# Kernel optimization log

Measured on AMD Instinct MI355X. Metric: run time of the kernel, lower is better.

The kernel has to match this reference:

```python
import jax, jax.numpy as jnp
import numpy as np

N_NODES = 100000


def gcn_conv(x, src, dst, dinv, W, b):
    # PyG GCNConv: h = D^-1/2 (A+I) D^-1/2 (x W) + b
    h = x @ W                                   # [N, out]
    norm = dinv[src] * dinv[dst]                # [E'] edge weights
    msg = norm[:, None] * h[src]                # gather + scale
    agg = jax.ops.segment_sum(msg, dst, num_segments=x.shape[0])
    return agg + b


def setup_inputs() -> dict:
    key = jax.random.key(0)
    ks = jax.random.split(key, 8)
    x = jax.random.normal(ks[0], (N_NODES, 64), dtype=jnp.float32)
    edge_index = jax.random.randint(ks[1], (2, 1600000), 0, N_NODES, dtype=jnp.int32)
    s = 0.1
    return {
        "x": x,
        "edge_index": edge_index,
        "W1": jax.random.normal(ks[2], (64, 64), dtype=jnp.float32) * s,
        "b1": jnp.zeros((64,), dtype=jnp.float32),
        "W2": jax.random.normal(ks[3], (64, 32), dtype=jnp.float32) * s,
        "b2": jnp.zeros((32,), dtype=jnp.float32),
        "W3": jax.random.normal(ks[4], (32, 2), dtype=jnp.float32) * s,
        "b3": jnp.zeros((2,), dtype=jnp.float32),
    }


def reference(x, edge_index, W1, b1, W2, b2, W3, b3):
    n = x.shape[0]
    loop = jnp.arange(n, dtype=edge_index.dtype)
    src = jnp.concatenate([edge_index[0], loop])  # add self-loops
    dst = jnp.concatenate([edge_index[1], loop])
    deg = jax.ops.segment_sum(jnp.ones_like(dst, dtype=x.dtype), dst, num_segments=n)
    dinv = jnp.where(deg > 0, jax.lax.rsqrt(jnp.maximum(deg, 1.0)), 0.0)
    h = jax.nn.relu(gcn_conv(x, src, dst, dinv, W1, b1))
    h = jax.nn.relu(gcn_conv(h, src, dst, dinv, W2, b2))
    return gcn_conv(h, src, dst, dinv, W3, b3)
```

## Files before the change

### kernel.cpp

```cpp
#include <hip/hip_runtime.h>
#include <hip/hip_fp16.h>

#define N_NODES 100000
#define N_EDGES 1600000
#define BSHIFT 9
#define NBUCK ((N_NODES + 511) / 512)
#define BCAP 12288

__global__ void bucket1_kernel(const int* __restrict__ src, const int* __restrict__ dst,
                               int* __restrict__ gbcount, int* __restrict__ bbuf, int E) {
    __shared__ int hcnt[NBUCK];
    __shared__ int hbase[NBUCK];
    int t = threadIdx.x;
    for (int i = t; i < NBUCK; i += 256) hcnt[i] = 0;
    __syncthreads();
    int e0 = blockIdx.x * 2048 + t;
    int ss[8], dd[8];
#pragma unroll
    for (int u = 0; u < 8; u++) {
        int e = e0 + u * 256;
        if (e < E) {
            ss[u] = src[e];
            dd[u] = dst[e];
            atomicAdd(&hcnt[dd[u] >> BSHIFT], 1);
        } else {
            dd[u] = -1;
        }
    }
    __syncthreads();
    for (int i = t; i < NBUCK; i += 256) {
        int c = hcnt[i];
        hbase[i] = c ? atomicAdd(&gbcount[i], c) : 0;
        hcnt[i] = 0;
    }
    __syncthreads();
#pragma unroll
    for (int u = 0; u < 8; u++) {
        if (dd[u] >= 0) {
            int bk = dd[u] >> BSHIFT;
            int r = atomicAdd(&hcnt[bk], 1);
            bbuf[(size_t)bk * BCAP + hbase[bk] + r] = ss[u] | ((dd[u] & 511) << 17);
        }
    }
}

__global__ void scan196_kernel(const int* __restrict__ gbcount, int* __restrict__ gbase,
                               int* __restrict__ rowptrN, int E) {
    __shared__ int s[256];
    int t = threadIdx.x;
    int v = (t < NBUCK) ? gbcount[t] : 0;
    s[t] = v;
    __syncthreads();
    for (int off = 1; off < 256; off <<= 1) {
        int u = (t >= off) ? s[t - off] : 0;
        __syncthreads();
        s[t] += u;
        __syncthreads();
    }
    if (t < NBUCK) gbase[t] = s[t] - v;
    if (t == 0) *rowptrN = E;
}

__global__ __launch_bounds__(512)
void bucket2_kernel(const int* __restrict__ bbuf, const int* __restrict__ gbcount,
                    const int* __restrict__ gbase, int* __restrict__ rowptr,
                    float* __restrict__ dinv, int* __restrict__ eidx, int N) {
    int b = blockIdx.x;
    int base_node = b << BSHIFT;
    int nn = min(512, N - base_node);
    int t = threadIdx.x;
    __shared__ int s[512];
    __shared__ int cur[512];
    s[t] = 0;
    __syncthreads();
    int sz = gbcount[b];
    const int* eb = bbuf + (size_t)b * BCAP;
    for (int j = t; j < sz; j += 512) atomicAdd(&s[((unsigned)eb[j]) >> 17], 1);
    __syncthreads();
    int myc = s[t];
    if (t < nn) dinv[base_node + t] = rsqrtf((float)myc + 1.0f);
    __syncthreads();
    for (int off = 1; off < 512; off <<= 1) {
        int u = (t >= off) ? s[t - off] : 0;
        __syncthreads();
        s[t] += u;
        __syncthreads();
    }
    int rp = gbase[b] + s[t] - myc;
    if (t < nn) rowptr[base_node + t] = rp;
    cur[t] = rp;
    __syncthreads();
    for (int j = t; j < sz; j += 512) {
        int e = eb[j];
        int pos = atomicAdd(&cur[((unsigned)e) >> 17], 1);
        eidx[pos] = e & 0x1FFFF;
    }
}

__global__ void sortrow_wave(const int* __restrict__ rowptr, int* __restrict__ eidx, int n) {
    int g = (blockIdx.x * blockDim.x + threadIdx.x) >> 6;
    int lane = threadIdx.x & 63;
    if (g >= n) return;
    int start = rowptr[g];
    int end = rowptr[g + 1];
    int len = end - start;
    if (len <= 1) return;

    if (len <= 64) {
        int v = (lane < len) ? eidx[start + lane] : 0x7fffffff;
#pragma unroll
        for (int k = 2; k <= 64; k <<= 1) {
#pragma unroll
            for (int j = k >> 1; j > 0; j >>= 1) {
                int partner = __shfl_xor(v, j, 64);
                bool up = ((lane & k) == 0);
                bool keepMin = (((lane & j) == 0) == up);
                int mn = min(v, partner), mx = max(v, partner);
                v = keepMin ? mn : mx;
            }
        }
        if (lane < len) eidx[start + lane] = v;
    } else if (lane == 0) {
        for (int i = start + 1; i < end; i++) {
            int key = eidx[i];
            int j = i - 1;
            while (j >= start && eidx[j] > key) { eidx[j + 1] = eidx[j]; j--; }
            eidx[j + 1] = key;
        }
    }
}

template <int FIN, int FOUT>
__global__ __launch_bounds__(256, 2)
void gemm_tiled(const float* __restrict__ in, const float* __restrict__ W,
                const float* __restrict__ dinv, __half* __restrict__ out, int n) {
    constexpr int CG = FOUT / 4;
    constexpr int RG = 256 / CG;
    constexpr int TR = RG * 4;
    constexpr int LDA = FIN + 4;
    __shared__ float sIn[TR * LDA];
    __shared__ float sW[FIN * FOUT];

    for (int i = threadIdx.x; i < FIN * FOUT / 4; i += 256)
        ((float4*)sW)[i] = ((const float4*)W)[i];

    int r0 = blockIdx.x * TR;
    for (int i = threadIdx.x; i < TR * FIN / 4; i += 256) {
        int rr = i / (FIN / 4);
        int cc = i % (FIN / 4);
        int gr = r0 + rr;
        float4 v = (gr < n) ? ((const float4*)in)[(size_t)gr * (FIN / 4) + cc]
                            : make_float4(0.f, 0.f, 0.f, 0.f);
        *(float4*)&sIn[rr * LDA + cc * 4] = v;
    }
    __syncthreads();

    int tc = threadIdx.x % CG;
    int tr = threadIdx.x / CG;
    int rbase = tr * 4, cbase = tc * 4;
    float acc[4][4] = {};

#pragma unroll 2
    for (int k = 0; k < FIN; k += 4) {
        float4 a[4], b[4];
#pragma unroll
        for (int i = 0; i < 4; i++) a[i] = *(float4*)&sIn[(rbase + i) * LDA + k];
#pragma unroll
        for (int kk = 0; kk < 4; kk++) b[kk] = *(float4*)&sW[(k + kk) * FOUT + cbase];
#pragma unroll
        for (int i = 0; i < 4; i++) {
            acc[i][0] += a[i].x * b[0].x + a[i].y * b[1].x + a[i].z * b[2].x + a[i].w * b[3].x;
            acc[i][1] += a[i].x * b[0].y + a[i].y * b[1].y + a[i].z * b[2].y + a[i].w * b[3].y;
            acc[i][2] += a[i].x * b[0].z + a[i].y * b[1].z + a[i].z * b[2].z + a[i].w * b[3].z;
            acc[i][3] += a[i].x * b[0].w + a[i].y * b[1].w + a[i].z * b[2].w + a[i].w * b[3].w;
        }
    }

#pragma unroll
    for (int i = 0; i < 4; i++) {
        int gr = r0 + rbase + i;
        if (gr < n) {
            float dv = dinv[gr];
            union { __half h[4]; uint2 u; } pk;
            pk.h[0] = __float2half_rn(dv * acc[i][0]);
            pk.h[1] = __float2half_rn(dv * acc[i][1]);
            pk.h[2] = __float2half_rn(dv * acc[i][2]);
            pk.h[3] = __float2half_rn(dv * acc[i][3]);
            *(uint2*)&out[(size_t)gr * FOUT + cbase] = pk.u;
        }
    }
}

__global__ __launch_bounds__(256, 4)
void agg_gemm64_kernel(const int* __restrict__ eidx, const int* __restrict__ rowptr,
                       const float* __restrict__ dinv, const __half* __restrict__ h,
                       const float* __restrict__ bias, const float* __restrict__ W,
                       __half* __restrict__ out, int n) {
    constexpr int FIN = 64, FOUT = 32;
    constexpr int L = 16;
    constexpr int PH = FIN / L;
    constexpr int NODES = 256 / L;
    constexpr int SVS = FIN + 1;
    using vh = _Float16 __attribute__((ext_vector_type(PH)));
    __shared__ float sW[FIN * FOUT];
    __shared__ float sv[NODES * SVS];

    for (int i = threadIdx.x; i < FIN * FOUT / 4; i += 256)
        ((float4*)sW)[i] = ((const float4*)W)[i];

    int g = (blockIdx.x * blockDim.x + threadIdx.x) / L;
    int lane = threadIdx.x % L;
    int slot = threadIdx.x / L;
    float di = 0.f;

    if (g < n) {
        int j = rowptr[g];
        int end = rowptr[g + 1];
        di = dinv[g];
        const __half* hb = h + lane * PH;

        float acc0[PH], acc1[PH];
#pragma unroll
        for (int q = 0; q < PH; q++) { acc0[q] = 0.f; acc1[q] = 0.f; }

        for (; j + 16 <= end; j += 16) {
            int s0 = eidx[j];
            int s1 = eidx[j + 1];
            int s2 = eidx[j + 2];
            int s3 = eidx[j + 3];
            int s4 = eidx[j + 4];
            int s5 = eidx[j + 5];
            int s6 = eidx[j + 6];
            int s7 = eidx[j + 7];
            vh v0 = *(const vh*)(hb + (size_t)s0 * FIN);
            vh v1 = *(const vh*)(hb + (size_t)s1 * FIN);
            vh v2 = *(const vh*)(hb + (size_t)s2 * FIN);
            vh v3 = *(const vh*)(hb + (size_t)s3 * FIN);
            vh v4 = *(const vh*)(hb + (size_t)s4 * FIN);
            vh v5 = *(const vh*)(hb + (size_t)s5 * FIN);
            vh v6 = *(const vh*)(hb + (size_t)s6 * FIN);
            vh v7 = *(const vh*)(hb + (size_t)s7 * FIN);
            int s8  = eidx[j + 8];
            int s9  = eidx[j + 9];
            int s10 = eidx[j + 10];
            int s11 = eidx[j + 11];
            int s12 = eidx[j + 12];
            int s13 = eidx[j + 13];
            int s14 = eidx[j + 14];
            int s15 = eidx[j + 15];
            vh v8  = *(const vh*)(hb + (size_t)s8  * FIN);
            vh v9  = *(const vh*)(hb + (size_t)s9  * FIN);
            vh v10 = *(const vh*)(hb + (size_t)s10 * FIN);
            vh v11 = *(const vh*)(hb + (size_t)s11 * FIN);
            vh v12 = *(const vh*)(hb + (size_t)s12 * FIN);
            vh v13 = *(const vh*)(hb + (size_t)s13 * FIN);
            vh v14 = *(const vh*)(hb + (size_t)s14 * FIN);
            vh v15 = *(const vh*)(hb + (size_t)s15 * FIN);
#pragma unroll
            for (int q = 0; q < PH; q++) {
                acc0[q] += (float)v0[q] + (float)v2[q];
                acc1[q] += (float)v1[q] + (float)v3[q];
                acc0[q] += (float)v4[q] + (float)v6[q];
                acc1[q] += (float)v5[q] + (float)v7[q];
            }
#pragma unroll
            for (int q = 0; q < PH; q++) {
                acc0[q] += (float)v8[q]  + (float)v10[q];
                acc1[q] += (float)v9[q]  + (float)v11[q];
                acc0[q] += (float)v12[q] + (float)v14[q];
                acc1[q] += (float)v13[q] + (float)v15[q];
            }
        }
        for (; j + 8 <= end; j += 8) {
            int s0 = eidx[j];
            int s1 = eidx[j + 1];
            int s2 = eidx[j + 2];
            int s3 = eidx[j + 3];
            int s4 = eidx[j + 4];
            int s5 = eidx[j + 5];
            int s6 = eidx[j + 6];
            int s7 = eidx[j + 7];
            vh v0 = *(const vh*)(hb + (size_t)s0 * FIN);
            vh v1 = *(const vh*)(hb + (size_t)s1 * FIN);
            vh v2 = *(const vh*)(hb + (size_t)s2 * FIN);
            vh v3 = *(const vh*)(hb + (size_t)s3 * FIN);
            vh v4 = *(const vh*)(hb + (size_t)s4 * FIN);
            vh v5 = *(const vh*)(hb + (size_t)s5 * FIN);
            vh v6 = *(const vh*)(hb + (size_t)s6 * FIN);
            vh v7 = *(const vh*)(hb + (size_t)s7 * FIN);
#pragma unroll
            for (int q = 0; q < PH; q++) {
                acc0[q] += (float)v0[q] + (float)v2[q];
                acc1[q] += (float)v1[q] + (float)v3[q];
                acc0[q] += (float)v4[q] + (float)v6[q];
                acc1[q] += (float)v5[q] + (float)v7[q];
            }
        }
        for (; j + 2 <= end; j += 2) {
            int s0 = eidx[j];
            int s1 = eidx[j + 1];
            vh v0 = *(const vh*)(hb + (size_t)s0 * FIN);
            vh v1 = *(const vh*)(hb + (size_t)s1 * FIN);
#pragma unroll
            for (int q = 0; q < PH; q++) { acc0[q] += (float)v0[q]; acc1[q] += (float)v1[q]; }
        }
        if (j < end) {
            vh v = *(const vh*)(hb + (size_t)eidx[j] * FIN);
#pragma unroll
            for (int q = 0; q < PH; q++) acc0[q] += (float)v[q];
        }

        vh sf = *(const vh*)(hb + (size_t)g * FIN);
        float* svn = &sv[slot * SVS + lane * PH];
#pragma unroll
        for (int q = 0; q < PH; q++) {
            float v = di * ((acc0[q] + acc1[q]) + (float)sf[q]) + bias[lane * PH + q];
            svn[q] = fmaxf(v, 0.f);
        }
    }
    __syncthreads();

    if (g < n) {
        const float* vn = &sv[slot * SVS];
        constexpr int PC = FOUT / L;
        float o0 = 0.f, o1 = 0.f;
        for (int k = 0; k < FIN; k++) {
            float vk = vn[k];
            float2 w = *(const float2*)&sW[k * FOUT + lane * PC];
            o0 += vk * w.x;
            o1 += vk * w.y;
        }
        union { __half h2[2]; unsigned u; } pk;
        pk.h2[0] = __float2half_rn(di * o0);
        pk.h2[1] = __float2half_rn(di * o1);
        *(unsigned*)&out[(size_t)g * FOUT + lane * PC] = pk.u;
    }
}

template <int FIN, int FOUT, bool OUT_HALF>
__global__ __launch_bounds__(256, 4)
void agg_gemm_kernel(const int* __restrict__ eidx, const int* __restrict__ rowptr,
                     const float* __restrict__ dinv, const __half* __restrict__ h,
                     const float* __restrict__ bias, const float* __restrict__ W,
                     void* __restrict__ outv, int n) {
    constexpr int L = 8;
    constexpr int PH = FIN / L;
    constexpr int NODES = 256 / L;
    constexpr int SVS = FIN + 1;
    using vh = _Float16 __attribute__((ext_vector_type(PH)));
    __shared__ float sW[FIN * FOUT];
    __shared__ float sv[NODES * SVS];

    for (int i = threadIdx.x; i < FIN * FOUT / 4; i += 256)
        ((float4*)sW)[i] = ((const float4*)W)[i];

    int g = (blockIdx.x * blockDim.x + threadIdx.x) / L;
    int lane = threadIdx.x % L;
    int slot = threadIdx.x / L;
    float di = 0.f;

    if (g < n) {
        int j = rowptr[g];
        int end = rowptr[g + 1];
        di = dinv[g];
        const __half* hb = h + lane * PH;

        float acc0[PH], acc1[PH];
#pragma unroll
        for (int q = 0; q < PH; q++) { acc0[q] = 0.f; acc1[q] = 0.f; }

        for (; j + 8 <= end; j += 8) {
            int s0 = eidx[j];
            int s1 = eidx[j + 1];
            int s2 = eidx[j + 2];
            int s3 = eidx[j + 3];
            int s4 = eidx[j + 4];
            int s5 = eidx[j + 5];
            int s6 = eidx[j + 6];
            int s7 = eidx[j + 7];
            vh v0 = *(const vh*)(hb + (size_t)s0 * FIN);
            vh v1 = *(const vh*)(hb + (size_t)s1 * FIN);
            vh v2 = *(const vh*)(hb + (size_t)s2 * FIN);
            vh v3 = *(const vh*)(hb + (size_t)s3 * FIN);
            vh v4 = *(const vh*)(hb + (size_t)s4 * FIN);
            vh v5 = *(const vh*)(hb + (size_t)s5 * FIN);
            vh v6 = *(const vh*)(hb + (size_t)s6 * FIN);
            vh v7 = *(const vh*)(hb + (size_t)s7 * FIN);
#pragma unroll
            for (int q = 0; q < PH; q++) {
                acc0[q] += (float)v0[q] + (float)v2[q];
                acc1[q] += (float)v1[q] + (float)v3[q];
                acc0[q] += (float)v4[q] + (float)v6[q];
                acc1[q] += (float)v5[q] + (float)v7[q];
            }
        }
        for (; j + 2 <= end; j += 2) {
            int s0 = eidx[j];
            int s1 = eidx[j + 1];
            vh v0 = *(const vh*)(hb + (size_t)s0 * FIN);
            vh v1 = *(const vh*)(hb + (size_t)s1 * FIN);
#pragma unroll
            for (int q = 0; q < PH; q++) { acc0[q] += (float)v0[q]; acc1[q] += (float)v1[q]; }
        }
        if (j < end) {
            vh v = *(const vh*)(hb + (size_t)eidx[j] * FIN);
#pragma unroll
            for (int q = 0; q < PH; q++) acc0[q] += (float)v[q];
        }

        vh sf = *(const vh*)(hb + (size_t)g * FIN);
        float* svn = &sv[slot * SVS + lane * PH];
#pragma unroll
        for (int q = 0; q < PH; q++) {
            float v = di * ((acc0[q] + acc1[q]) + (float)sf[q]) + bias[lane * PH + q];
            svn[q] = fmaxf(v, 0.f);
        }
    }
    __syncthreads();

    if (g < n) {
        const float* vn = &sv[slot * SVS];
        if constexpr (OUT_HALF) {
            constexpr int PC = FOUT / L;
            float o[PC] = {};
            for (int k = 0; k < FIN; k++) {
                float vk = vn[k];
                float4 w = *(const float4*)&sW[k * FOUT + lane * PC];
                o[0] += vk * w.x; o[1] += vk * w.y; o[2] += vk * w.z; o[3] += vk * w.w;
            }
            union { __half h[4]; uint2 u; } pk;
#pragma unroll
            for (int q = 0; q < PC; q++) pk.h[q] = __float2half_rn(di * o[q]);
            *(uint2*)((__half*)outv + (size_t)g * FOUT + lane * PC) = pk.u;
        } else {
            if (lane < FOUT) {
                float o = 0.f;
                for (int k = 0; k < FIN; k++) o += vn[k] * sW[k * FOUT + lane];
                ((float*)outv)[(size_t)g * FOUT + lane] = di * o;
            }
        }
    }
}

__global__ void agg2_kernel(const int* __restrict__ eidx, const int* __restrict__ rowptr,
                            const float* __restrict__ dinv, const float* __restrict__ h,
                            const float* __restrict__ b, float* __restrict__ out, int n) {
    int g = blockIdx.x * blockDim.x + threadIdx.x;
    if (g >= n) return;
    const float2* h2 = (const float2*)h;
    int j = rowptr[g];
    int end = rowptr[g + 1];
    float di = dinv[g];
    float2 hs = h2[g];

    float2 a0 = {0.f, 0.f}, a1 = {0.f, 0.f}, a2 = {0.f, 0.f}, a3 = {0.f, 0.f};
    float2 a4 = {0.f, 0.f}, a5 = {0.f, 0.f}, a6 = {0.f, 0.f}, a7 = {0.f, 0.f};
    for (; j + 8 <= end; j += 8) {
        int s0 = eidx[j];
        int s1 = eidx[j + 1];
        int s2 = eidx[j + 2];
        int s3 = eidx[j + 3];
        int s4 = eidx[j + 4];
        int s5 = eidx[j + 5];
        int s6 = eidx[j + 6];
        int s7 = eidx[j + 7];
        float2 v0 = h2[s0]; float2 v1 = h2[s1];
        float2 v2 = h2[s2]; float2 v3 = h2[s3];
        float2 v4 = h2[s4]; float2 v5 = h2[s5];
        float2 v6 = h2[s6]; float2 v7 = h2[s7];
        a0.x += v0.x; a0.y += v0.y;  a1.x += v1.x; a1.y += v1.y;
        a2.x += v2.x; a2.y += v2.y;  a3.x += v3.x; a3.y += v3.y;
        a4.x += v4.x; a4.y += v4.y;  a5.x += v5.x; a5.y += v5.y;
        a6.x += v6.x; a6.y += v6.y;  a7.x += v7.x; a7.y += v7.y;
    }
    for (; j + 2 <= end; j += 2) {
        float2 v0 = h2[eidx[j]];
        float2 v1 = h2[eidx[j + 1]];
        a0.x += v0.x; a0.y += v0.y;
        a1.x += v1.x; a1.y += v1.y;
    }
    if (j < end) {
        float2 v = h2[eidx[j]];
        a2.x += v.x; a2.y += v.y;
    }
    float accx = ((a0.x + a1.x) + (a2.x + a3.x)) + ((a4.x + a5.x) + (a6.x + a7.x));
    float accy = ((a0.y + a1.y) + (a2.y + a3.y)) + ((a4.y + a5.y) + (a6.y + a7.y));
    float2 r;
    r.x = di * (accx + hs.x) + b[0];
    r.y = di * (accy + hs.y) + b[1];
    ((float2*)out)[g] = r;
}

extern "C" void kernel_launch(void* const* d_in, const int* in_sizes, int n_in,
                              void* d_out, int out_size, void* d_ws, size_t ws_size,
                              hipStream_t stream) {
    const float* x  = (const float*)d_in[0];
    const int* ei   = (const int*)d_in[1];
    const float* W1 = (const float*)d_in[2];
    const float* b1 = (const float*)d_in[3];
    const float* W2 = (const float*)d_in[4];
    const float* b2 = (const float*)d_in[5];
    const float* W3 = (const float*)d_in[6];
    const float* b3 = (const float*)d_in[7];
    float* out = (float*)d_out;

    const int N = N_NODES;
    const int E = N_EDGES;
    const int* src = ei;
    const int* dst = ei + E;

    char* p = (char*)d_ws;
    int*    rowptr  = (int*)p;            p += ((size_t)(N + 1) * 4 + 15) / 16 * 16;
    float*  dinv    = (float*)p;          p += ((size_t)N * 4 + 15) / 16 * 16;
    int*    gbcount = (int*)p;            p += ((size_t)NBUCK * 4 + 15) / 16 * 16;
    int*    gbase   = (int*)p;            p += ((size_t)NBUCK * 4 + 15) / 16 * 16;
    int*    eidx    = (int*)p;            p += (size_t)E * 4;
    __half* A1      = (__half*)p;         p += (size_t)N * 64 * 2;
    __half* A2      = (__half*)p;         p += (size_t)N * 32 * 2;
    float*  A3      = (float*)p;          p += (size_t)N * 2 * 4;
    int*    bbuf    = (int*)p;

    const int T = 256;

    hipMemsetAsync(gbcount, 0, NBUCK * sizeof(int), stream);
    bucket1_kernel<<<(E + 2047) / 2048, T, 0, stream>>>(src, dst, gbcount, bbuf, E);
    scan196_kernel<<<1, 256, 0, stream>>>(gbcount, gbase, rowptr + N, E);
    bucket2_kernel<<<NBUCK, 512, 0, stream>>>(bbuf, gbcount, gbase, rowptr, dinv, eidx, N);
    sortrow_wave<<<(N * 64 + T - 1) / T, T, 0, stream>>>(rowptr, eidx, N);

    gemm_tiled<64, 64><<<(N + 63) / 64, T, 0, stream>>>(x, W1, dinv, A1, N);

    agg_gemm64_kernel<<<(N + 15) / 16, T, 0, stream>>>(
        eidx, rowptr, dinv, A1, b1, W2, A2, N);

    agg_gemm_kernel<32, 2, false><<<(N + 31) / 32, T, 0, stream>>>(
        eidx, rowptr, dinv, A2, b2, W3, A3, N);

    agg2_kernel<<<(N + T - 1) / T, T, 0, stream>>>(eidx, rowptr, dinv, A3, b3, out, N);
}
```

Measured before the change: 272.2 us.

## Use finer destination buckets and narrower lane groups in aggregation kernels

Bucket width drops from 512 to 256 nodes, which doubles the bucket count, halves the per-bucket buffer capacity and widens the bucket scan to 512 threads. The bucket2 kernel keeps 512 threads but only 256 of them do the per-node scan. In the layer-2 aggregation each node now uses 8 lanes instead of 16, so each lane gathers 8 halves, 32 nodes fit per block, and the 16-edge unroll is removed. Layer 3 becomes a dedicated FIN=32 kernel with 4 lanes per node. The aim is to cut idle lanes and raise gather width per thread, at the risk of lower memory-level parallelism per node and bucket overflow if degree skew grows.

```diff
diff --git a/kernel.cpp b/kernel.cpp
--- a/kernel.cpp
+++ b/kernel.cpp
@@ -3,9 +3,9 @@
 
 #define N_NODES 100000
 #define N_EDGES 1600000
-#define BSHIFT 9
-#define NBUCK ((N_NODES + 511) / 512)
-#define BCAP 12288
+#define BSHIFT 8
+#define NBUCK ((N_NODES + 255) / 256)
+#define BCAP 6144
 
 __global__ void bucket1_kernel(const int* __restrict__ src, const int* __restrict__ dst,
                                int* __restrict__ gbcount, int* __restrict__ bbuf, int E) {
@@ -39,19 +39,20 @@
         if (dd[u] >= 0) {
             int bk = dd[u] >> BSHIFT;
             int r = atomicAdd(&hcnt[bk], 1);
-            bbuf[(size_t)bk * BCAP + hbase[bk] + r] = ss[u] | ((dd[u] & 511) << 17);
-        }
-    }
-}
-
-__global__ void scan196_kernel(const int* __restrict__ gbcount, int* __restrict__ gbase,
-                               int* __restrict__ rowptrN, int E) {
-    __shared__ int s[256];
+            bbuf[(size_t)bk * BCAP + hbase[bk] + r] = ss[u] | ((dd[u] & 255) << 17);
+        }
+    }
+}
+
+__global__ __launch_bounds__(512)
+void scan_buckets_kernel(const int* __restrict__ gbcount, int* __restrict__ gbase,
+                         int* __restrict__ rowptrN, int E) {
+    __shared__ int s[512];
     int t = threadIdx.x;
     int v = (t < NBUCK) ? gbcount[t] : 0;
     s[t] = v;
     __syncthreads();
-    for (int off = 1; off < 256; off <<= 1) {
+    for (int off = 1; off < 512; off <<= 1) {
         int u = (t >= off) ? s[t - off] : 0;
         __syncthreads();
         s[t] += u;
@@ -67,28 +68,30 @@
                     float* __restrict__ dinv, int* __restrict__ eidx, int N) {
     int b = blockIdx.x;
     int base_node = b << BSHIFT;
-    int nn = min(512, N - base_node);
+    int nn = min(256, N - base_node);
     int t = threadIdx.x;
-    __shared__ int s[512];
-    __shared__ int cur[512];
-    s[t] = 0;
+    __shared__ int s[256];
+    __shared__ int cur[256];
+    if (t < 256) s[t] = 0;
     __syncthreads();
     int sz = gbcount[b];
     const int* eb = bbuf + (size_t)b * BCAP;
     for (int j = t; j < sz; j += 512) atomicAdd(&s[((unsigned)eb[j]) >> 17], 1);
     __syncthreads();
-    int myc = s[t];
+    int myc = (t < 256) ? s[t] : 0;
     if (t < nn) dinv[base_node + t] = rsqrtf((float)myc + 1.0f);
     __syncthreads();
-    for (int off = 1; off < 512; off <<= 1) {
-        int u = (t >= off) ? s[t - off] : 0;
+    for (int off = 1; off < 256; off <<= 1) {
+        int u = (t >= off && t < 256) ? s[t - off] : 0;
         __syncthreads();
-        s[t] += u;
+        if (t < 256) s[t] += u;
         __syncthreads();
     }
-    int rp = gbase[b] + s[t] - myc;
-    if (t < nn) rowptr[base_node + t] = rp;
-    cur[t] = rp;
+    if (t < 256) {
+        int rp = gbase[b] + s[t] - myc;
+        if (t < nn) rowptr[base_node + t] = rp;
+        cur[t] = rp;
+    }
     __syncthreads();
     for (int j = t; j < sz; j += 512) {
         int e = eb[j];
@@ -197,7 +200,7 @@
                        const float* __restrict__ bias, const float* __restrict__ W,
                        __half* __restrict__ out, int n) {
     constexpr int FIN = 64, FOUT = 32;
-    constexpr int L = 16;
+    constexpr int L = 8;
     constexpr int PH = FIN / L;
     constexpr int NODES = 256 / L;
     constexpr int SVS = FIN + 1;
@@ -223,54 +226,6 @@
 #pragma unroll
         for (int q = 0; q < PH; q++) { acc0[q] = 0.f; acc1[q] = 0.f; }
 
-        for (; j + 16 <= end; j += 16) {
-            int s0 = eidx[j];
-            int s1 = eidx[j + 1];
-            int s2 = eidx[j + 2];
-            int s3 = eidx[j + 3];
-            int s4 = eidx[j + 4];
-            int s5 = eidx[j + 5];
-            int s6 = eidx[j + 6];
-            int s7 = eidx[j + 7];
-            vh v0 = *(const vh*)(hb + (size_t)s0 * FIN);
-            vh v1 = *(const vh*)(hb + (size_t)s1 * FIN);
-            vh v2 = *(const vh*)(hb + (size_t)s2 * FIN);
-            vh v3 = *(const vh*)(hb + (size_t)s3 * FIN);
-            vh v4 = *(const vh*)(hb + (size_t)s4 * FIN);
-            vh v5 = *(const vh*)(hb + (size_t)s5 * FIN);
-            vh v6 = *(const vh*)(hb + (size_t)s6 * FIN);
-            vh v7 = *(const vh*)(hb + (size_t)s7 * FIN);
-            int s8  = eidx[j + 8];
-            int s9  = eidx[j + 9];
-            int s10 = eidx[j + 10];
-            int s11 = eidx[j + 11];
-            int s12 = eidx[j + 12];
-            int s13 = eidx[j + 13];
-            int s14 = eidx[j + 14];
-            int s15 = eidx[j + 15];
-            vh v8  = *(const vh*)(hb + (size_t)s8  * FIN);
-            vh v9  = *(const vh*)(hb + (size_t)s9  * FIN);
-            vh v10 = *(const vh*)(hb + (size_t)s10 * FIN);
-            vh v11 = *(const vh*)(hb + (size_t)s11 * FIN);
-            vh v12 = *(const vh*)(hb + (size_t)s12 * FIN);
-            vh v13 = *(const vh*)(hb + (size_t)s13 * FIN);
-            vh v14 = *(const vh*)(hb + (size_t)s14 * FIN);
-            vh v15 = *(const vh*)(hb + (size_t)s15 * FIN);
-#pragma unroll
-            for (int q = 0; q < PH; q++) {
-                acc0[q] += (float)v0[q] + (float)v2[q];
-                acc1[q] += (float)v1[q] + (float)v3[q];
-                acc0[q] += (float)v4[q] + (float)v6[q];
-                acc1[q] += (float)v5[q] + (float)v7[q];
-            }
-#pragma unroll
-            for (int q = 0; q < PH; q++) {
-                acc0[q] += (float)v8[q]  + (float)v10[q];
-                acc1[q] += (float)v9[q]  + (float)v11[q];
-                acc0[q] += (float)v12[q] + (float)v14[q];
-                acc1[q] += (float)v13[q] + (float)v15[q];
-            }
-        }
         for (; j + 8 <= end; j += 8) {
             int s0 = eidx[j];
             int s1 = eidx[j + 1];
@@ -323,27 +278,26 @@
     if (g < n) {
         const float* vn = &sv[slot * SVS];
         constexpr int PC = FOUT / L;
-        float o0 = 0.f, o1 = 0.f;
+        float o[PC] = {};
         for (int k = 0; k < FIN; k++) {
             float vk = vn[k];
-            float2 w = *(const float2*)&sW[k * FOUT + lane * PC];
-            o0 += vk * w.x;
-            o1 += vk * w.y;
-        }
-        union { __half h2[2]; unsigned u; } pk;
-        pk.h2[0] = __float2half_rn(di * o0);
-        pk.h2[1] = __float2half_rn(di * o1);
-        *(unsigned*)&out[(size_t)g * FOUT + lane * PC] = pk.u;
-    }
-}
-
-template <int FIN, int FOUT, bool OUT_HALF>
+            float4 w = *(const float4*)&sW[k * FOUT + lane * PC];
+            o[0] += vk * w.x; o[1] += vk * w.y; o[2] += vk * w.z; o[3] += vk * w.w;
+        }
+        union { __half h2[4]; uint2 u; } pk;
+#pragma unroll
+        for (int q = 0; q < PC; q++) pk.h2[q] = __float2half_rn(di * o[q]);
+        *(uint2*)&out[(size_t)g * FOUT + lane * PC] = pk.u;
+    }
+}
+
 __global__ __launch_bounds__(256, 4)
-void agg_gemm_kernel(const int* __restrict__ eidx, const int* __restrict__ rowptr,
-                     const float* __restrict__ dinv, const __half* __restrict__ h,
-                     const float* __restrict__ bias, const float* __restrict__ W,
-                     void* __restrict__ outv, int n) {
-    constexpr int L = 8;
+void agg_gemm32_kernel(const int* __restrict__ eidx, const int* __restrict__ rowptr,
+                       const float* __restrict__ dinv, const __half* __restrict__ h,
+                       const float* __restrict__ bias, const float* __restrict__ W,
+                       float* __restrict__ out, int n) {
+    constexpr int FIN = 32, FOUT = 2;
+    constexpr int L = 4;
     constexpr int PH = FIN / L;
     constexpr int NODES = 256 / L;
     constexpr int SVS = FIN + 1;
@@ -351,8 +305,7 @@
     __shared__ float sW[FIN * FOUT];
     __shared__ float sv[NODES * SVS];
 
-    for (int i = threadIdx.x; i < FIN * FOUT / 4; i += 256)
-        ((float4*)sW)[i] = ((const float4*)W)[i];
+    if (threadIdx.x < FIN * FOUT) sW[threadIdx.x] = W[threadIdx.x];
 
     int g = (blockIdx.x * blockDim.x + threadIdx.x) / L;
     int lane = threadIdx.x % L;
@@ -418,27 +371,11 @@
     }
     __syncthreads();
 
-    if (g < n) {
+    if (g < n && lane < FOUT) {
         const float* vn = &sv[slot * SVS];
-        if constexpr (OUT_HALF) {
-            constexpr int PC = FOUT / L;
-            float o[PC] = {};
-            for (int k = 0; k < FIN; k++) {
-                float vk = vn[k];
-                float4 w = *(const float4*)&sW[k * FOUT + lane * PC];
-                o[0] += vk * w.x; o[1] += vk * w.y; o[2] += vk * w.z; o[3] += vk * w.w;
-            }
-            union { __half h[4]; uint2 u; } pk;
-#pragma unroll
-            for (int q = 0; q < PC; q++) pk.h[q] = __float2half_rn(di * o[q]);
-            *(uint2*)((__half*)outv + (size_t)g * FOUT + lane * PC) = pk.u;
-        } else {
-            if (lane < FOUT) {
-                float o = 0.f;
-                for (int k = 0; k < FIN; k++) o += vn[k] * sW[k * FOUT + lane];
-                ((float*)outv)[(size_t)g * FOUT + lane] = di * o;
-            }
-        }
+        float o = 0.f;
+        for (int k = 0; k < FIN; k++) o += vn[k] * sW[k * FOUT + lane];
+        out[(size_t)g * FOUT + lane] = di * o;
     }
 }
 
@@ -524,16 +461,16 @@
 
     hipMemsetAsync(gbcount, 0, NBUCK * sizeof(int), stream);
     bucket1_kernel<<<(E + 2047) / 2048, T, 0, stream>>>(src, dst, gbcount, bbuf, E);
-    scan196_kernel<<<1, 256, 0, stream>>>(gbcount, gbase, rowptr + N, E);
+    scan_buckets_kernel<<<1, 512, 0, stream>>>(gbcount, gbase, rowptr + N, E);
     bucket2_kernel<<<NBUCK, 512, 0, stream>>>(bbuf, gbcount, gbase, rowptr, dinv, eidx, N);
     sortrow_wave<<<(N * 64 + T - 1) / T, T, 0, stream>>>(rowptr, eidx, N);
 
     gemm_tiled<64, 64><<<(N + 63) / 64, T, 0, stream>>>(x, W1, dinv, A1, N);
 
-    agg_gemm64_kernel<<<(N + 15) / 16, T, 0, stream>>>(
+    agg_gemm64_kernel<<<(N + 31) / 32, T, 0, stream>>>(
         eidx, rowptr, dinv, A1, b1, W2, A2, N);
 
-    agg_gemm_kernel<32, 2, false><<<(N + 31) / 32, T, 0, stream>>>(
+    agg_gemm32_kernel<<<(N + 63) / 64, T, 0, stream>>>(
         eidx, rowptr, dinv, A2, b2, W3, A3, N);
 
     agg2_kernel<<<(N + T - 1) / T, T, 0, stream>>>(eidx, rowptr, dinv, A3, b3, out, N);
```

After: 275.7 us. Within noise of the previous version (+1.3%).
